# Kernel optimization log

Measured on AMD Instinct MI355X. Metric: run time of the kernel, lower is better.

The kernel has to match this reference:

```python
import jax, jax.numpy as jnp
import numpy as np

B = 1048576
D = 64
N_CLASSES = 10


def setup_inputs() -> dict:
    key = jax.random.key(0)
    k1, k2, k3, k4, k5, k6 = jax.random.split(key, 6)
    return {
        "anchor_output": jax.random.normal(k1, (B, D), dtype=jnp.float32),
        "positive_output": jax.random.normal(k2, (B, D), dtype=jnp.float32),
        "negative_output": jax.random.normal(k3, (B, D), dtype=jnp.float32),
        "anchor_label": jax.random.randint(k4, (B,), 0, N_CLASSES, dtype=jnp.int64) if jax.config.jax_enable_x64 else jax.random.randint(k4, (B,), 0, N_CLASSES, dtype=jnp.int32),
        "negative_label": jax.random.randint(k5, (B,), 0, N_CLASSES, dtype=jnp.int32),
        "margin_matrix": jax.random.uniform(k6, (N_CLASSES, N_CLASSES), dtype=jnp.float32),
    }


def reference(anchor_output, positive_output, negative_output, anchor_label, negative_label, margin_matrix):
    # squared euclidean distances per sample: [B]
    distance_positive = jnp.sum(jnp.square(anchor_output - positive_output), axis=1)
    distance_negative = jnp.sum(jnp.square(anchor_output - negative_output), axis=1)
    # vectorized gather of per-pair margins: [B]
    margin = margin_matrix[anchor_label, negative_label]
    losses = jax.nn.relu(distance_positive - distance_negative + margin)
    return jnp.mean(losses)
```

## Files before the change

### kernel.cpp

```cpp
#include <hip/hip_runtime.h>


namespace {
constexpr int kB           = 1048576;
constexpr int kNC          = 10;
constexpr int kBlock       = 256;
constexpr int kLanesPerRow = 16;
constexpr int kRowsPerBlk  = kBlock / kLanesPerRow;
constexpr int kUnroll      = 2;
constexpr int kRowsPerIter = kRowsPerBlk * kUnroll;
constexpr int kGrid        = 2048;

typedef float vfloat4 __attribute__((ext_vector_type(4)));
}

__global__ __launch_bounds__(kBlock) void triplet_partial_kernel(
    const vfloat4* __restrict__ a,
    const vfloat4* __restrict__ p,
    const vfloat4* __restrict__ n,
    const int*     __restrict__ alab,
    const int*     __restrict__ nlab,
    const float*   __restrict__ mm,
    float*         __restrict__ partials)
{
    __shared__ float s_m[kNC * kNC];
    for (int i = threadIdx.x; i < kNC * kNC; i += kBlock) s_m[i] = mm[i];
    __syncthreads();

    const int j   = threadIdx.x & (kLanesPerRow - 1);
    const int rib = threadIdx.x / kLanesPerRow;

    float acc = 0.0f;

    #pragma unroll 1
    for (int base = blockIdx.x * kRowsPerIter; base < kB;
         base += kGrid * kRowsPerIter) {
        const int r0 = base + rib;

        vfloat4 av[kUnroll], pv[kUnroll], nv[kUnroll];
        #pragma unroll
        for (int u = 0; u < kUnroll; ++u) {
            const int idx = (r0 + u * kRowsPerBlk) * kLanesPerRow + j;
            av[u] = a[idx];
            pv[u] = __builtin_nontemporal_load(&p[idx]);
            nv[u] = __builtin_nontemporal_load(&n[idx]);
        }

        int al[kUnroll], nl[kUnroll];
        if (j == 0) {
            #pragma unroll
            for (int u = 0; u < kUnroll; ++u) {
                const int r = r0 + u * kRowsPerBlk;
                al[u] = alab[r];
                nl[u] = nlab[r];
            }
        }

        float diff[kUnroll];
        #pragma unroll
        for (int u = 0; u < kUnroll; ++u) {
            float d, dp = 0.0f, dn = 0.0f;
            d = av[u].x - pv[u].x; dp = fmaf(d, d, dp);
            d = av[u].y - pv[u].y; dp = fmaf(d, d, dp);
            d = av[u].z - pv[u].z; dp = fmaf(d, d, dp);
            d = av[u].w - pv[u].w; dp = fmaf(d, d, dp);
            d = av[u].x - nv[u].x; dn = fmaf(d, d, dn);
            d = av[u].y - nv[u].y; dn = fmaf(d, d, dn);
            d = av[u].z - nv[u].z; dn = fmaf(d, d, dn);
            d = av[u].w - nv[u].w; dn = fmaf(d, d, dn);
            diff[u] = dp - dn;
        }

        #pragma unroll
        for (int m = 8; m >= 1; m >>= 1) {
            #pragma unroll
            for (int u = 0; u < kUnroll; ++u)
                diff[u] += __shfl_xor(diff[u], m, 64);
        }

        if (j == 0) {
            #pragma unroll
            for (int u = 0; u < kUnroll; ++u) {
                const float loss = diff[u] + s_m[al[u] * kNC + nl[u]];
                acc += (loss > 0.0f) ? loss : 0.0f;
            }
        }
    }

    #pragma unroll
    for (int m = 32; m >= 1; m >>= 1) acc += __shfl_xor(acc, m, 64);
    __shared__ float s_red[kBlock / 64];
    if ((threadIdx.x & 63) == 0) s_red[threadIdx.x >> 6] = acc;
    __syncthreads();
    if (threadIdx.x == 0) {
        float s = 0.0f;
        #pragma unroll
        for (int w = 0; w < kBlock / 64; ++w) s += s_red[w];
        partials[blockIdx.x] = s;
    }
}

__global__ __launch_bounds__(256) void triplet_finalize_kernel(
    const float* __restrict__ partials, float* __restrict__ out, int g)
{
    float acc = 0.0f;
    for (int i = threadIdx.x; i < g; i += 256) acc += partials[i];
    #pragma unroll
    for (int m = 32; m >= 1; m >>= 1) acc += __shfl_xor(acc, m, 64);
    __shared__ float s_red[4];
    if ((threadIdx.x & 63) == 0) s_red[threadIdx.x >> 6] = acc;
    __syncthreads();
    if (threadIdx.x == 0) {
        out[0] = (s_red[0] + s_red[1] + s_red[2] + s_red[3]) * (1.0f / (float)kB);
    }
}

extern "C" void kernel_launch(void* const* d_in, const int* in_sizes, int n_in,
                              void* d_out, int out_size, void* d_ws, size_t ws_size,
                              hipStream_t stream) {
    const vfloat4* a    = (const vfloat4*)d_in[0];
    const vfloat4* p    = (const vfloat4*)d_in[1];
    const vfloat4* n    = (const vfloat4*)d_in[2];
    const int*     alab = (const int*)d_in[3];
    const int*     nlab = (const int*)d_in[4];
    const float*   mm   = (const float*)d_in[5];

    float* partials = (float*)d_ws;
    float* out      = (float*)d_out;

    triplet_partial_kernel<<<kGrid, kBlock, 0, stream>>>(a, p, n, alab, nlab, mm, partials);
    triplet_finalize_kernel<<<1, 256, 0, stream>>>(partials, out, kGrid);
}
```

Before: 125.4 us.

## Fuse final reduction into main kernel via last-block atomic counter

Removes the separate finalize kernel launch. Each block now bumps an atomic counter after writing its partial, and the last block to arrive reduces all partials and writes the mean. It also doubles the grid to 4096 blocks. In exchange it adds a memset of the counter before each launch, a threadfence plus atomic per block, and a serial tail reduction inside the last block.

```diff
diff --git a/kernel.cpp b/kernel.cpp
--- a/kernel.cpp
+++ b/kernel.cpp
@@ -9,19 +9,21 @@
 constexpr int kRowsPerBlk  = kBlock / kLanesPerRow;
 constexpr int kUnroll      = 2;
 constexpr int kRowsPerIter = kRowsPerBlk * kUnroll;
-constexpr int kGrid        = 2048;
+constexpr int kGrid        = 4096;
 
 typedef float vfloat4 __attribute__((ext_vector_type(4)));
 }
 
-__global__ __launch_bounds__(kBlock) void triplet_partial_kernel(
+__global__ __launch_bounds__(kBlock) void triplet_fused_kernel(
     const vfloat4* __restrict__ a,
     const vfloat4* __restrict__ p,
     const vfloat4* __restrict__ n,
     const int*     __restrict__ alab,
     const int*     __restrict__ nlab,
     const float*   __restrict__ mm,
-    float*         __restrict__ partials)
+    float*         __restrict__ partials,
+    unsigned int*  __restrict__ counter,
+    float*         __restrict__ out)
 {
     __shared__ float s_m[kNC * kNC];
     for (int i = threadIdx.x; i < kNC * kNC; i += kBlock) s_m[i] = mm[i];
@@ -90,6 +92,7 @@
     #pragma unroll
     for (int m = 32; m >= 1; m >>= 1) acc += __shfl_xor(acc, m, 64);
     __shared__ float s_red[kBlock / 64];
+    __shared__ bool  s_last;
     if ((threadIdx.x & 63) == 0) s_red[threadIdx.x >> 6] = acc;
     __syncthreads();
     if (threadIdx.x == 0) {
@@ -97,21 +100,24 @@
         #pragma unroll
         for (int w = 0; w < kBlock / 64; ++w) s += s_red[w];
         partials[blockIdx.x] = s;
+        __threadfence();
+        const unsigned int old = atomicAdd(counter, 1u);
+        s_last = (old == (unsigned int)(kGrid - 1));
     }
-}
+    __syncthreads();
 
-__global__ __launch_bounds__(256) void triplet_finalize_kernel(
-    const float* __restrict__ partials, float* __restrict__ out, int g)
-{
-    float acc = 0.0f;
-    for (int i = threadIdx.x; i < g; i += 256) acc += partials[i];
-    #pragma unroll
-    for (int m = 32; m >= 1; m >>= 1) acc += __shfl_xor(acc, m, 64);
-    __shared__ float s_red[4];
-    if ((threadIdx.x & 63) == 0) s_red[threadIdx.x >> 6] = acc;
-    __syncthreads();
-    if (threadIdx.x == 0) {
-        out[0] = (s_red[0] + s_red[1] + s_red[2] + s_red[3]) * (1.0f / (float)kB);
+    if (s_last) {
+        __threadfence();
+        float facc = 0.0f;
+        #pragma unroll 1
+        for (int i = threadIdx.x; i < kGrid; i += kBlock) facc += partials[i];
+        #pragma unroll
+        for (int m = 32; m >= 1; m >>= 1) facc += __shfl_xor(facc, m, 64);
+        if ((threadIdx.x & 63) == 0) s_red[threadIdx.x >> 6] = facc;
+        __syncthreads();
+        if (threadIdx.x == 0) {
+            out[0] = (s_red[0] + s_red[1] + s_red[2] + s_red[3]) * (1.0f / (float)kB);
+        }
     }
 }
 
@@ -125,9 +131,12 @@
     const int*     nlab = (const int*)d_in[4];
     const float*   mm   = (const float*)d_in[5];
 
-    float* partials = (float*)d_ws;
-    float* out      = (float*)d_out;
+    float*        partials = (float*)d_ws;
+    unsigned int* counter  = (unsigned int*)((char*)d_ws + kGrid * sizeof(float));
+    float*        out      = (float*)d_out;
 
-    triplet_partial_kernel<<<kGrid, kBlock, 0, stream>>>(a, p, n, alab, nlab, mm, partials);
-    triplet_finalize_kernel<<<1, 256, 0, stream>>>(partials, out, kGrid);
+    hipMemsetAsync(counter, 0, sizeof(unsigned int), stream);
+
+    triplet_fused_kernel<<<kGrid, kBlock, 0, stream>>>(
+        a, p, n, alab, nlab, mm, partials, counter, out);
 }
```

Measured after the change: 325.9 us. 160% more time.
